# Optimization experiments

Measured on AMD Instinct MI355X. Metric: run time of the kernel, lower is better.

The kernel has to match this reference:

```python
import jax, jax.numpy as jnp
import numpy as np

D_MODEL = 1024
NUM_HEADS = 16
HEAD_DIM = D_MODEL // NUM_HEADS
SCALE = HEAD_DIM ** -0.5
ROPE_BASE = 10000.0


def _rope_cos_sin(seq_len, dim, dtype=jnp.float32):
    inv_freq = 1.0 / (ROPE_BASE ** (jnp.arange(0, dim, 2, dtype=jnp.float32) / dim))
    t = jnp.arange(seq_len, dtype=jnp.float32)
    freqs = t[:, None] * inv_freq[None, :]            # [S, dim/2]
    emb = jnp.concatenate([freqs, freqs], axis=-1)    # [S, dim]
    # broadcast shape [1, S, 1, dim] to apply over [B, S, H, dim]
    return emb.astype(dtype)[None, :, None, :]


def _rotate_half(x):
    half = x.shape[-1] // 2
    x1, x2 = x[..., :half], x[..., half:]
    return jnp.concatenate([-x2, x1], axis=-1)


def setup_inputs() -> dict:
    key = jax.random.key(0)
    ks = jax.random.split(key, 5)
    B, S = 2, 2048
    x = jax.random.normal(ks[0], (B, S, D_MODEL), dtype=jnp.float32)
    wq = jax.random.normal(ks[1], (D_MODEL, D_MODEL), dtype=jnp.float32) * (D_MODEL ** -0.5)
    wk = jax.random.normal(ks[2], (D_MODEL, D_MODEL), dtype=jnp.float32) * (D_MODEL ** -0.5)
    wv = jax.random.normal(ks[3], (D_MODEL, D_MODEL), dtype=jnp.float32) * (D_MODEL ** -0.5)
    wo = jax.random.normal(ks[4], (D_MODEL, D_MODEL), dtype=jnp.float32) * (D_MODEL ** -0.5)
    attention_mask = jnp.tril(jnp.ones((S, S), dtype=jnp.int32))  # causal
    return {"x": x, "wq": wq, "wk": wk, "wv": wv, "wo": wo,
            "attention_mask": attention_mask}


def reference(x, wq, wk, wv, wo, attention_mask):
    B, S, _ = x.shape
    # projections (nn.Linear, no bias: y = x @ W^T)
    q = (x @ wq.T).reshape(B, S, NUM_HEADS, HEAD_DIM)
    k = (x @ wk.T).reshape(B, S, NUM_HEADS, HEAD_DIM)
    v = (x @ wv.T).reshape(B, S, NUM_HEADS, HEAD_DIM)
    # RoPE
    emb = _rope_cos_sin(S, HEAD_DIM, x.dtype)
    cos, sin = jnp.cos(emb), jnp.sin(emb)
    q = q * cos + _rotate_half(q) * sin
    k = k * cos + _rotate_half(k) * sin
    # attention scores [B, H, S, S]
    scores = jnp.einsum('bihd,bjhd->bhij', q, k) * SCALE
    mask = attention_mask[None, None, :, :]  # 2D mask -> broadcast over batch, heads
    scores = jnp.where(mask == 0, -jnp.inf, scores)
    attn = jax.nn.softmax(scores, axis=-1)
    attn = jnp.nan_to_num(attn, nan=0.0)  # fully-masked rows -> 0
    out = jnp.einsum('bhij,bjhd->bihd', attn, v).reshape(B, S, D_MODEL)
    return out @ wo.T
```

## Files before the change

kernel.cpp:

```cpp
#include <hip/hip_runtime.h>

typedef __bf16 bf16;
typedef __attribute__((ext_vector_type(8))) __bf16 bf16x8;
typedef __attribute__((ext_vector_type(4))) float f32x4;
typedef __attribute__((ext_vector_type(4))) short s16x4;
typedef __attribute__((ext_vector_type(4))) unsigned u32x4;

#define SEQ 2048
#define DM 1024
#define NH 16
#define HD 64
#define QSCALE 0.1803368801111204f

static __device__ __forceinline__ void gl_lds16(const bf16* g, bf16* l) {
  __builtin_amdgcn_global_load_lds(
      (const __attribute__((address_space(1))) void*)g,
      (__attribute__((address_space(3))) void*)l, 16, 0, 0);
}

static __device__ __forceinline__ f32x4 mfma16(bf16x8 a, bf16x8 b, f32x4 c) {
  return __builtin_amdgcn_mfma_f32_16x16x32_bf16(a, b, c, 0, 0, 0);
}

static __device__ __forceinline__ unsigned cvt_pk_bf16(float lo, float hi) {
  unsigned r;
  asm("v_cvt_pk_bf16_f32 %0, %1, %2" : "=v"(r) : "v"(lo), "v"(hi));
  return r;
}

__global__ __launch_bounds__(256)
void prep_k(const float* __restrict__ x, const float* __restrict__ wq,
            const float* __restrict__ wk, const float* __restrict__ wv,
            const float* __restrict__ wo, bf16* __restrict__ xb,
            bf16* __restrict__ wb, float* __restrict__ tab) {
  int i = blockIdx.x * 256 + threadIdx.x;
  if (i < 2097152) {
    const float* src;
    bf16* dst;
    int j;
    if (i < 1048576) {
      src = x; dst = xb; j = i;
    } else {
      j = i - 1048576;
      int seg = j >> 18;
      src = (seg == 0) ? wq : (seg == 1) ? wk : (seg == 2) ? wv : wo;
      dst = wb;
      src -= (size_t)seg << 20;
    }
    f32x4 v = ((const f32x4*)src)[j];
    s16x4 o;
#pragma unroll
    for (int q = 0; q < 4; ++q) o[q] = __builtin_bit_cast(short, (bf16)v[q]);
    ((s16x4*)dst)[j] = o;
  } else {
    int idx = i - 2097152;
    int s = idx >> 5, j = idx & 31;
    float inv = powf(10000.0f, -(float)j * (1.0f / 32.0f));
    float f = (float)s * inv;
    tab[idx * 2] = cosf(f);
    tab[idx * 2 + 1] = sinf(f);
  }
}

__global__ __launch_bounds__(256)
void gemm_qkv(const bf16* __restrict__ A, const bf16* __restrict__ B,
              bf16* __restrict__ qh, bf16* __restrict__ kh, bf16* __restrict__ vt,
              const float2* __restrict__ tab) {
  const int K = 1024;
  __shared__ __attribute__((aligned(16))) bf16 As[128 * 32];
  __shared__ __attribute__((aligned(16))) bf16 Bs[128 * 32];
  const int t = threadIdx.x;
  const int wv = t >> 6, ln = t & 63, lr = ln & 15, lg = ln >> 4;
  const int wr = wv >> 1, wc = wv & 1;
  const int m0 = blockIdx.y * 128, n0 = blockIdx.x * 128;
  const int srow = t >> 2, sslot = t & 3;
  const int seg = n0 >> 10;
  const int hh = ((n0 & 1023) + wc * 64) >> 6;

  f32x4 acc[4][4] = {};

  for (int kt = 0; kt < K; kt += 32) {
#pragma unroll
    for (int c = 0; c < 2; ++c) {
      int row = srow + (c << 6);
      int lsl = sslot ^ (row & 3);
      gl_lds16(A + (size_t)(m0 + row) * K + kt + lsl * 8, As + c * 2048 + wv * 512);
      gl_lds16(B + (size_t)(n0 + row) * K + kt + lsl * 8, Bs + c * 2048 + wv * 512);
    }
    __syncthreads();
    bf16x8 af[4], bfr[4];
#pragma unroll
    for (int i = 0; i < 4; ++i) {
      int ra = wr * 64 + i * 16 + lr;
      af[i] = *(const bf16x8*)(As + ra * 32 + ((lg ^ (ra & 3)) << 3));
      int rb = wc * 64 + i * 16 + lr;
      bfr[i] = *(const bf16x8*)(Bs + rb * 32 + ((lg ^ (rb & 3)) << 3));
    }
#pragma unroll
    for (int i = 0; i < 4; ++i)
#pragma unroll
      for (int j = 0; j < 4; ++j)
        acc[i][j] = mfma16(af[i], bfr[j], acc[i][j]);
    __syncthreads();
  }

#pragma unroll
  for (int i = 0; i < 4; ++i) {
    int row0 = m0 + wr * 64 + i * 16 + lg * 4;
    int bb = row0 >> 11, s0r = row0 & (SEQ - 1);
    if (seg < 2) {
      bf16* dst = (seg == 0) ? qh : kh;
      float scl = (seg == 0) ? QSCALE : 1.0f;
      size_t base = ((size_t)(bb * NH + hh) * SEQ + s0r) * HD;
#pragma unroll
      for (int j = 0; j < 2; ++j) {
        int dlo = j * 16 + lr;
#pragma unroll
        for (int r = 0; r < 4; ++r) {
          float2 cs = tab[(size_t)(s0r + r) * 32 + dlo];
          float a = acc[i][j][r], b2 = acc[i][j + 2][r];
          float na = (a * cs.x - b2 * cs.y) * scl;
          float nb = (b2 * cs.x + a * cs.y) * scl;
          dst[base + (size_t)r * HD + dlo] = (bf16)na;
          dst[base + (size_t)r * HD + dlo + 32] = (bf16)nb;
        }
      }
    } else {
#pragma unroll
      for (int j = 0; j < 4; ++j) {
        int d = j * 16 + lr;
        s16x4 pk;
#pragma unroll
        for (int r = 0; r < 4; ++r) pk[r] = __builtin_bit_cast(short, (bf16)acc[i][j][r]);
        *(s16x4*)(vt + ((size_t)(bb * NH + hh) * HD + d) * SEQ + s0r) = pk;
      }
    }
  }
}

__global__ __launch_bounds__(256)
void gemm_bt_f32(const bf16* __restrict__ A, const bf16* __restrict__ B,
                 float* __restrict__ C, int M, int N, int K) {
  __shared__ __attribute__((aligned(16))) bf16 As[128 * 32];
  __shared__ __attribute__((aligned(16))) bf16 Bs[128 * 32];
  const int t = threadIdx.x;
  const int wv = t >> 6, ln = t & 63, lr = ln & 15, lg = ln >> 4;
  const int wr = wv >> 1, wc = wv & 1;
  const int m0 = blockIdx.y * 128, n0 = blockIdx.x * 128;
  const int srow = t >> 2, sslot = t & 3;

  f32x4 acc[4][4] = {};

  for (int kt = 0; kt < K; kt += 32) {
#pragma unroll
    for (int c = 0; c < 2; ++c) {
      int row = srow + (c << 6);
      int lsl = sslot ^ (row & 3);
      gl_lds16(A + (size_t)(m0 + row) * K + kt + lsl * 8, As + c * 2048 + wv * 512);
      gl_lds16(B + (size_t)(n0 + row) * K + kt + lsl * 8, Bs + c * 2048 + wv * 512);
    }
    __syncthreads();
    bf16x8 af[4], bfr[4];
#pragma unroll
    for (int i = 0; i < 4; ++i) {
      int ra = wr * 64 + i * 16 + lr;
      af[i] = *(const bf16x8*)(As + ra * 32 + ((lg ^ (ra & 3)) << 3));
      int rb = wc * 64 + i * 16 + lr;
      bfr[i] = *(const bf16x8*)(Bs + rb * 32 + ((lg ^ (rb & 3)) << 3));
    }
#pragma unroll
    for (int i = 0; i < 4; ++i)
#pragma unroll
      for (int j = 0; j < 4; ++j)
        acc[i][j] = mfma16(af[i], bfr[j], acc[i][j]);
    __syncthreads();
  }

#pragma unroll
  for (int i = 0; i < 4; ++i) {
    int row0 = m0 + wr * 64 + i * 16 + lg * 4;
#pragma unroll
    for (int j = 0; j < 4; ++j) {
      int col = n0 + wc * 64 + j * 16 + lr;
#pragma unroll
      for (int r = 0; r < 4; ++r)
        C[(size_t)(row0 + r) * N + col] = acc[i][j][r];
    }
  }
}

template <bool MASKED>
static __device__ __forceinline__ void attn_tile_lds(
    const bf16* Ksb, const bf16* Vsb, unsigned* plw,
    const bf16x8* qf, f32x4* acc, float& m_run, float& l_run,
    int lr, int lg, int qrow, int s0) {
  f32x4 sc[4] = {};
#pragma unroll
  for (int fi = 0; fi < 4; ++fi) {
    int row = fi * 16 + lr;
    int sw = row & 7;
    bf16x8 k0 = *(const bf16x8*)(Ksb + row * 64 + ((lg ^ sw) << 3));
    bf16x8 k1 = *(const bf16x8*)(Ksb + row * 64 + (((4 + lg) ^ sw) << 3));
    sc[fi] = mfma16(k0, qf[0], sc[fi]);
    sc[fi] = mfma16(k1, qf[1], sc[fi]);
  }
  if (MASKED) {
#pragma unroll
    for (int fi = 0; fi < 4; ++fi)
#pragma unroll
      for (int r = 0; r < 4; ++r) {
        int kv = s0 + fi * 16 + lg * 4 + r;
        sc[fi][r] = (kv <= qrow) ? sc[fi][r] : -3e38f;
      }
  }
  float mx = sc[0][0];
#pragma unroll
  for (int fi = 0; fi < 4; ++fi)
#pragma unroll
    for (int r = 0; r < 4; ++r) mx = fmaxf(mx, sc[fi][r]);
  mx = fmaxf(mx, __shfl_xor(mx, 16));
  mx = fmaxf(mx, __shfl_xor(mx, 32));
  float mn = fmaxf(m_run, mx);
  float alpha = __builtin_amdgcn_exp2f(m_run - mn);
  m_run = mn;
  float pf[4][4], sm = 0.0f;
#pragma unroll
  for (int fi = 0; fi < 4; ++fi)
#pragma unroll
    for (int r = 0; r < 4; ++r) {
      pf[fi][r] = __builtin_amdgcn_exp2f(sc[fi][r] - mn);
      sm += pf[fi][r];
    }
  sm += __shfl_xor(sm, 16);
  sm += __shfl_xor(sm, 32);
  l_run = l_run * alpha + sm;
#pragma unroll
  for (int d0 = 0; d0 < 4; ++d0)
#pragma unroll
    for (int r = 0; r < 4; ++r) acc[d0][r] *= alpha;

  const int sw2 = (lr & 7) << 2;
#pragma unroll
  for (int fi = 0; fi < 4; ++fi)
#pragma unroll
    for (int hh = 0; hh < 2; ++hh)
      plw[lr * 32 + ((fi * 8 + lg * 2 + hh) ^ sw2)] =
          cvt_pk_bf16(pf[fi][2 * hh], pf[fi][2 * hh + 1]);
  asm volatile("s_waitcnt lgkmcnt(0)" ::: "memory");
  __builtin_amdgcn_sched_barrier(0);
#pragma unroll
  for (int kc = 0; kc < 2; ++kc) {
    u32x4 praw = *(const u32x4*)(plw + lr * 32 + ((kc * 16 + lg * 4) ^ sw2));
    bf16x8 pb = __builtin_bit_cast(bf16x8, praw);
#pragma unroll
    for (int d0 = 0; d0 < 4; ++d0) {
      int row = d0 * 16 + lr;
      int sw = row & 7;
      bf16x8 vf = *(const bf16x8*)(Vsb + row * 64 + (((kc * 4 + lg) ^ sw) << 3));
      acc[d0] = mfma16(vf, pb, acc[d0]);
    }
  }
  asm volatile("" ::: "memory");
}

__global__ __launch_bounds__(256, 2)
void attn_k(const bf16* __restrict__ qh, const bf16* __restrict__ kh,
            const bf16* __restrict__ vt, bf16* __restrict__ ao) {
  __shared__ __attribute__((aligned(16))) bf16 Ks[2][64 * 64];
  __shared__ __attribute__((aligned(16))) bf16 Vs[2][64 * 64];
  __shared__ __attribute__((aligned(16))) unsigned plds[4][512];

  const int t = threadIdx.x, wv = t >> 6, ln = t & 63, lr = ln & 15, lg = ln >> 4;
  const int bid = blockIdx.x;
  const int xcd = bid & 7, rest = bid >> 3;
  const int bh = xcd * 4 + (rest >> 4);
  const int p = rest & 15;
  const int b = bh >> 4, h = bh & 15;
  const int qtA = 31 - p, qtB = p;

  const bf16* qp = qh + (size_t)bh * SEQ * HD;
  const bf16* kp = kh + (size_t)bh * SEQ * HD;
  const bf16* vp = vt + (size_t)bh * HD * SEQ;
  unsigned* plw = &plds[wv][0];

  const int qrowA = qtA * 64 + wv * 16 + lr;
  const int qrowB = qtB * 64 + wv * 16 + lr;

  bf16x8 qfA[2], qfB[2];
  qfA[0] = *(const bf16x8*)(qp + (size_t)qrowA * HD + lg * 8);
  qfA[1] = *(const bf16x8*)(qp + (size_t)qrowA * HD + 32 + lg * 8);
  qfB[0] = *(const bf16x8*)(qp + (size_t)qrowB * HD + lg * 8);
  qfB[1] = *(const bf16x8*)(qp + (size_t)qrowB * HD + 32 + lg * 8);

  f32x4 accA[4] = {}, accB[4] = {};
  float mA = -3e38f, lA = 0.0f, mB = -3e38f, lB = 0.0f;

  const int nt = qtA + 1;

  auto STAGE = [&](int buf, int tt) {
    int s0 = tt * 64;
#pragma unroll
    for (int c = 0; c < 2; ++c) {
      int rA = wv * 16 + c * 8;
      int row = rA + (ln >> 3);
      int sl = (ln & 7) ^ (row & 7);
      gl_lds16(kp + (size_t)(s0 + row) * HD + (sl << 3), &Ks[buf][rA * 64]);
      gl_lds16(vp + (size_t)row * SEQ + s0 + (sl << 3), &Vs[buf][rA * 64]);
    }
  };

  STAGE(0, 0);
  asm volatile("s_waitcnt vmcnt(0)" ::: "memory");
  __builtin_amdgcn_s_barrier();

  int cur = 0;
  for (int tt = 0; tt < nt; ++tt) {
    if (tt + 1 < nt) STAGE(cur ^ 1, tt + 1);
    if (tt == qtA)
      attn_tile_lds<true>(&Ks[cur][0], &Vs[cur][0], plw, qfA, accA, mA, lA, lr, lg, qrowA, tt * 64);
    else
      attn_tile_lds<false>(&Ks[cur][0], &Vs[cur][0], plw, qfA, accA, mA, lA, lr, lg, qrowA, tt * 64);
    if (tt <= qtB) {
      if (tt == qtB)
        attn_tile_lds<true>(&Ks[cur][0], &Vs[cur][0], plw, qfB, accB, mB, lB, lr, lg, qrowB, tt * 64);
      else
        attn_tile_lds<false>(&Ks[cur][0], &Vs[cur][0], plw, qfB, accB, mB, lB, lr, lg, qrowB, tt * 64);
    }
    asm volatile("s_waitcnt vmcnt(0)" ::: "memory");
    __builtin_amdgcn_s_barrier();
    cur ^= 1;
  }

#pragma unroll
  for (int ph = 0; ph < 2; ++ph) {
    f32x4* acc = ph ? accB : accA;
    float invl = 1.0f / (ph ? lB : lA);
    int qrow = ph ? qrowB : qrowA;
    bf16* aop = ao + ((size_t)b * SEQ + qrow) * DM + h * HD;
#pragma unroll
    for (int d0 = 0; d0 < 4; ++d0) {
      unsigned lo = cvt_pk_bf16(acc[d0][0] * invl, acc[d0][1] * invl);
      unsigned hi = cvt_pk_bf16(acc[d0][2] * invl, acc[d0][3] * invl);
      uint2 pk; pk.x = lo; pk.y = hi;
      *(uint2*)(aop + d0 * 16 + lg * 4) = pk;
    }
  }
}

extern "C" void kernel_launch(void* const* d_in, const int* in_sizes, int n_in,
                              void* d_out, int out_size, void* d_ws, size_t ws_size,
                              hipStream_t stream) {
  const float* x = (const float*)d_in[0];
  const float* wq = (const float*)d_in[1];
  const float* wk = (const float*)d_in[2];
  const float* wv = (const float*)d_in[3];
  const float* wo = (const float*)d_in[4];

  char* ws = (char*)d_ws;
  const size_t MB = 1ull << 20;
  bf16* xb    = (bf16*)ws;
  bf16* wqkvb = (bf16*)(ws + 8 * MB);
  bf16* wob   = (bf16*)(ws + 14 * MB);
  bf16* qhb   = (bf16*)(ws + 16 * MB);
  bf16* khb   = (bf16*)(ws + 24 * MB);
  bf16* vtb   = (bf16*)(ws + 32 * MB);
  float* tab  = (float*)(ws + 40 * MB);
  bf16* aob = xb;

  prep_k<<<8448, 256, 0, stream>>>(x, wq, wk, wv, wo, xb, wqkvb, tab);

  gemm_qkv<<<dim3(24, 32), 256, 0, stream>>>(xb, wqkvb, qhb, khb, vtb, (const float2*)tab);

  attn_k<<<512, 256, 0, stream>>>(qhb, khb, vtb, aob);

  gemm_bt_f32<<<dim3(8, 32), 256, 0, stream>>>(aob, wob, (float*)d_out, 4096, 1024, 1024);
}
```

Measured before the change: 124.4 us.

## Split paired q-tiles into one tile per block and skip redundant softmax rescale

The attention kernel used to process two causal q-tiles per block (a long and a short one paired for balance). It now launches 1024 blocks with one q-tile each, ordered longest first, and raises the occupancy hint to 4 blocks per CU. The online softmax also skips the alpha rescale of the accumulators when no row maximum grew anywhere in the wave, and uses a tree max reduction. This trades the built-in load balancing of the pairing for more parallelism and occupancy, and K/V tiles are now loaded once per q-tile instead of shared by two.

```diff
diff --git a/kernel.cpp b/kernel.cpp
--- a/kernel.cpp
+++ b/kernel.cpp
@@ -26,6 +26,10 @@
   unsigned r;
   asm("v_cvt_pk_bf16_f32 %0, %1, %2" : "=v"(r) : "v"(lo), "v"(hi));
   return r;
+}
+
+static __device__ __forceinline__ float vmax4(f32x4 v) {
+  return fmaxf(fmaxf(v[0], v[1]), fmaxf(v[2], v[3]));
 }
 
 __global__ __launch_bounds__(256)
@@ -213,31 +217,31 @@
         sc[fi][r] = (kv <= qrow) ? sc[fi][r] : -3e38f;
       }
   }
-  float mx = sc[0][0];
-#pragma unroll
-  for (int fi = 0; fi < 4; ++fi)
-#pragma unroll
-    for (int r = 0; r < 4; ++r) mx = fmaxf(mx, sc[fi][r]);
+  float mx = fmaxf(fmaxf(vmax4(sc[0]), vmax4(sc[1])),
+                   fmaxf(vmax4(sc[2]), vmax4(sc[3])));
   mx = fmaxf(mx, __shfl_xor(mx, 16));
   mx = fmaxf(mx, __shfl_xor(mx, 32));
-  float mn = fmaxf(m_run, mx);
-  float alpha = __builtin_amdgcn_exp2f(m_run - mn);
-  m_run = mn;
+  if (!__all(mx <= m_run)) {
+    float mn = fmaxf(m_run, mx);
+    float alpha = __builtin_amdgcn_exp2f(m_run - mn);
+    m_run = mn;
+    l_run *= alpha;
+#pragma unroll
+    for (int d0 = 0; d0 < 4; ++d0)
+#pragma unroll
+      for (int r = 0; r < 4; ++r) acc[d0][r] *= alpha;
+  }
   float pf[4][4], sm = 0.0f;
 #pragma unroll
   for (int fi = 0; fi < 4; ++fi)
 #pragma unroll
     for (int r = 0; r < 4; ++r) {
-      pf[fi][r] = __builtin_amdgcn_exp2f(sc[fi][r] - mn);
+      pf[fi][r] = __builtin_amdgcn_exp2f(sc[fi][r] - m_run);
       sm += pf[fi][r];
     }
   sm += __shfl_xor(sm, 16);
   sm += __shfl_xor(sm, 32);
-  l_run = l_run * alpha + sm;
-#pragma unroll
-  for (int d0 = 0; d0 < 4; ++d0)
-#pragma unroll
-    for (int r = 0; r < 4; ++r) acc[d0][r] *= alpha;
+  l_run += sm;
 
   const int sw2 = (lr & 7) << 2;
 #pragma unroll
@@ -263,7 +267,7 @@
   asm volatile("" ::: "memory");
 }
 
-__global__ __launch_bounds__(256, 2)
+__global__ __launch_bounds__(256, 4)
 void attn_k(const bf16* __restrict__ qh, const bf16* __restrict__ kh,
             const bf16* __restrict__ vt, bf16* __restrict__ ao) {
   __shared__ __attribute__((aligned(16))) bf16 Ks[2][64 * 64];
@@ -272,30 +276,26 @@
 
   const int t = threadIdx.x, wv = t >> 6, ln = t & 63, lr = ln & 15, lg = ln >> 4;
   const int bid = blockIdx.x;
-  const int xcd = bid & 7, rest = bid >> 3;
-  const int bh = xcd * 4 + (rest >> 4);
-  const int p = rest & 15;
+  const int xcd = bid & 7, g = bid >> 3;
+  const int bh = xcd * 4 + (g & 3);
+  const int qt = 31 - (g >> 2);
   const int b = bh >> 4, h = bh & 15;
-  const int qtA = 31 - p, qtB = p;
 
   const bf16* qp = qh + (size_t)bh * SEQ * HD;
   const bf16* kp = kh + (size_t)bh * SEQ * HD;
   const bf16* vp = vt + (size_t)bh * HD * SEQ;
   unsigned* plw = &plds[wv][0];
 
-  const int qrowA = qtA * 64 + wv * 16 + lr;
-  const int qrowB = qtB * 64 + wv * 16 + lr;
-
-  bf16x8 qfA[2], qfB[2];
-  qfA[0] = *(const bf16x8*)(qp + (size_t)qrowA * HD + lg * 8);
-  qfA[1] = *(const bf16x8*)(qp + (size_t)qrowA * HD + 32 + lg * 8);
-  qfB[0] = *(const bf16x8*)(qp + (size_t)qrowB * HD + lg * 8);
-  qfB[1] = *(const bf16x8*)(qp + (size_t)qrowB * HD + 32 + lg * 8);
-
-  f32x4 accA[4] = {}, accB[4] = {};
-  float mA = -3e38f, lA = 0.0f, mB = -3e38f, lB = 0.0f;
-
-  const int nt = qtA + 1;
+  const int qrow = qt * 64 + wv * 16 + lr;
+
+  bf16x8 qf[2];
+  qf[0] = *(const bf16x8*)(qp + (size_t)qrow * HD + lg * 8);
+  qf[1] = *(const bf16x8*)(qp + (size_t)qrow * HD + 32 + lg * 8);
+
+  f32x4 acc[4] = {};
+  float m_run = -3e38f, l_run = 0.0f;
+
+  const int nt = qt + 1;
 
   auto STAGE = [&](int buf, int tt) {
     int s0 = tt * 64;
@@ -316,34 +316,25 @@
   int cur = 0;
   for (int tt = 0; tt < nt; ++tt) {
     if (tt + 1 < nt) STAGE(cur ^ 1, tt + 1);
-    if (tt == qtA)
-      attn_tile_lds<true>(&Ks[cur][0], &Vs[cur][0], plw, qfA, accA, mA, lA, lr, lg, qrowA, tt * 64);
+    if (tt == qt)
+      attn_tile_lds<true>(&Ks[cur][0], &Vs[cur][0], plw, qf, acc, m_run, l_run,
+                          lr, lg, qrow, tt * 64);
     else
-      attn_tile_lds<false>(&Ks[cur][0], &Vs[cur][0], plw, qfA, accA, mA, lA, lr, lg, qrowA, tt * 64);
-    if (tt <= qtB) {
-      if (tt == qtB)
-        attn_tile_lds<true>(&Ks[cur][0], &Vs[cur][0], plw, qfB, accB, mB, lB, lr, lg, qrowB, tt * 64);
-      else
-        attn_tile_lds<false>(&Ks[cur][0], &Vs[cur][0], plw, qfB, accB, mB, lB, lr, lg, qrowB, tt * 64);
-    }
+      attn_tile_lds<false>(&Ks[cur][0], &Vs[cur][0], plw, qf, acc, m_run, l_run,
+                           lr, lg, qrow, tt * 64);
     asm volatile("s_waitcnt vmcnt(0)" ::: "memory");
     __builtin_amdgcn_s_barrier();
     cur ^= 1;
   }
 
-#pragma unroll
-  for (int ph = 0; ph < 2; ++ph) {
-    f32x4* acc = ph ? accB : accA;
-    float invl = 1.0f / (ph ? lB : lA);
-    int qrow = ph ? qrowB : qrowA;
-    bf16* aop = ao + ((size_t)b * SEQ + qrow) * DM + h * HD;
-#pragma unroll
-    for (int d0 = 0; d0 < 4; ++d0) {
-      unsigned lo = cvt_pk_bf16(acc[d0][0] * invl, acc[d0][1] * invl);
-      unsigned hi = cvt_pk_bf16(acc[d0][2] * invl, acc[d0][3] * invl);
-      uint2 pk; pk.x = lo; pk.y = hi;
-      *(uint2*)(aop + d0 * 16 + lg * 4) = pk;
-    }
+  float invl = 1.0f / l_run;
+  bf16* aop = ao + ((size_t)b * SEQ + qrow) * DM + h * HD;
+#pragma unroll
+  for (int d0 = 0; d0 < 4; ++d0) {
+    unsigned lo = cvt_pk_bf16(acc[d0][0] * invl, acc[d0][1] * invl);
+    unsigned hi = cvt_pk_bf16(acc[d0][2] * invl, acc[d0][3] * invl);
+    uint2 pk; pk.x = lo; pk.y = hi;
+    *(uint2*)(aop + d0 * 16 + lg * 4) = pk;
   }
 }
 
@@ -371,7 +362,7 @@
 
   gemm_qkv<<<dim3(24, 32), 256, 0, stream>>>(xb, wqkvb, qhb, khb, vtb, (const float2*)tab);
 
-  attn_k<<<512, 256, 0, stream>>>(qhb, khb, vtb, aob);
+  attn_k<<<1024, 256, 0, stream>>>(qhb, khb, vtb, aob);
 
   gemm_bt_f32<<<dim3(8, 32), 256, 0, stream>>>(aob, wob, (float*)d_out, 4096, 1024, 1024);
 }
```

Result: faster. 119.4 us (-4.0%).
